# Performance work log

Measured on AMD Instinct MI355X. Metric: run time of the kernel, lower is better.

The kernel has to match this reference:

```python
import jax, jax.numpy as jnp
import numpy as np

N = 50000          # nodes
E = 1600000        # edges (avg degree 32)
IN = 256
OUT = 16
HEADS = 8
NEG_SLOPE = 0.2


def setup_inputs() -> dict:
    key = jax.random.key(0)
    k1, k2, k3, k4, k5, k6 = jax.random.split(key, 6)
    row = jax.random.randint(k1, (E,), 0, N)            # destination node of each edge
    col = jax.random.randint(k2, (E,), 0, N)            # source node of each edge
    h = jax.random.normal(k3, (N, IN), dtype=jnp.float32)
    # xavier-uniform-like scales
    w_scale = float(np.sqrt(6.0 / (IN + OUT * HEADS)))
    a_scale = float(np.sqrt(6.0 / (HEADS * OUT + 1)))
    W = jax.random.uniform(k4, (IN, OUT * HEADS), jnp.float32, -w_scale, w_scale)
    a_l = jax.random.uniform(k5, (1, HEADS, OUT), jnp.float32, -a_scale, a_scale)
    a_r = jax.random.uniform(k6, (1, HEADS, OUT), jnp.float32, -a_scale, a_scale)
    return {"row": row, "col": col, "h": h, "W": W, "a_l": a_l, "a_r": a_r}


def reference(row, col, h, W, a_l, a_r):
    n = h.shape[0]
    heads, out = a_l.shape[1], a_l.shape[2]
    Wh = (h @ W).reshape(n, heads, out)                 # [N, H, D]
    Wh1 = (Wh * a_l).sum(2)                             # [N, H]
    Wh2 = (Wh * a_r).sum(2)                             # [N, H]
    e = Wh1[row] + Wh2[col]                             # [E, H]
    e = jnp.where(e > 0, e, NEG_SLOPE * e)              # leaky relu
    # segment (row-wise) softmax over edges sharing the same destination row
    m = jax.ops.segment_max(e, row, num_segments=n)     # [N, H]
    ex = jnp.exp(e - m[row])                            # [E, H]
    s = jax.ops.segment_sum(ex, row, num_segments=n)    # [N, H]
    alpha = ex / s[row]                                 # [E, H]
    # torch .reshape(-1, out, heads) reinterprets memory layout (NOT a transpose)
    Wh_r = Wh.reshape(n, out, heads)                    # [N, D, H]
    msg = alpha[:, None, :] * Wh_r[col]                 # [E, D, H]
    h_prime = jax.ops.segment_sum(msg, row, num_segments=n)  # [N, D, H]
    return jax.nn.relu(h_prime)
```

## Files before the change

### kernel.cpp

```cpp
#include <hip/hip_runtime.h>
#include <cfloat>
#include <math.h>


constexpr int IN_F  = 256;
constexpr int F     = 128;
constexpr int HEADS = 8;
constexpr int BS    = 32;
constexpr int BSH   = 5;
constexpr int SLAB  = 2048;
constexpr int CSLAB = 9216;
constexpr int PTILE = 4096;

typedef __attribute__((ext_vector_type(8))) short bf16x8;
typedef __attribute__((ext_vector_type(4))) float f32x4;

__device__ inline uint f2bf(float x) {
    uint u = __float_as_uint(x);
    return (u + 0x7fffu + ((u >> 16) & 1u)) >> 16;
}
__device__ inline uint pack2(float a, float b) { return f2bf(a) | (f2bf(b) << 16); }

__global__ __launch_bounds__(256) void prepack(const float* __restrict__ W,
                                               uint4* __restrict__ Wf,
                                               int* __restrict__ cursorC,
                                               int* __restrict__ cursorF,
                                               int NC, int NBF)
{
    if (blockIdx.x == 0) {
        for (int i = threadIdx.x; i < NC; i += 256) cursorC[i] = i * CSLAB;
        for (int i = threadIdx.x; i < NBF; i += 256) cursorF[i] = i * SLAB;
    }
    int t = blockIdx.x * 256 + threadIdx.x;
    if (t >= 8 * 8 * 64) return;
    int ks = t >> 9, nt = (t >> 6) & 7, l = t & 63;
    int col = nt * 16 + (l & 15);
    int k0 = ks * 32 + (l >> 4) * 8;
    float v[8];
#pragma unroll
    for (int i = 0; i < 8; ++i) v[i] = W[(size_t)(k0 + i) * F + col];
    Wf[t] = make_uint4(pack2(v[0], v[1]), pack2(v[2], v[3]),
                       pack2(v[4], v[5]), pack2(v[6], v[7]));
}

__global__ __launch_bounds__(256) void gemm_push(
    const float* __restrict__ h, const uint4* __restrict__ Wf,
    const float* __restrict__ a_l, const float* __restrict__ a_r,
    uint* __restrict__ Whb, float* __restrict__ Wh1, float* __restrict__ Wh2,
    int n, int NGEMM,
    const int* __restrict__ row, const int* __restrict__ col,
    int* __restrict__ cursorC, uint* __restrict__ cpairs, int E)
{
    __shared__ uint stage[PTILE];
    __shared__ int hist[256], st[256], cur[256], gbase[256];
    const int tid = threadIdx.x;

    if (blockIdx.x >= NGEMM) {
        const int t = tid;
        const int i0 = (blockIdx.x - NGEMM) * PTILE;
        const int cnt = min(PTILE, E - i0);
        hist[t] = 0;
        __syncthreads();

        uint u[PTILE / 256];
#pragma unroll
        for (int j = 0; j < PTILE / 256; ++j) {
            const int idx = t + j * 256;
            if (idx < cnt) {
                int r = row[i0 + idx], c = col[i0 + idx];
                u[j] = ((uint)(r >> 8) << 24) | ((uint)c << 8) | (uint)(r & 255);
                atomicAdd(&hist[r >> 8], 1);
            } else u[j] = 0xFFFFFFFFu;
        }
        __syncthreads();

        const int v = hist[t];
        st[t] = v;
        __syncthreads();
        for (int off = 1; off < 256; off <<= 1) {
            int x = (t >= off) ? st[t - off] : 0;
            __syncthreads();
            st[t] += x;
            __syncthreads();
        }
        cur[t] = st[t] - v;
        if (v) gbase[t] = atomicAdd(&cursorC[t], v);
        __syncthreads();

#pragma unroll
        for (int j = 0; j < PTILE / 256; ++j) {
            if (u[j] != 0xFFFFFFFFu) {
                int k = u[j] >> 24;
                int pos = atomicAdd(&cur[k], 1);
                stage[pos] = u[j];
            }
        }
        __syncthreads();

        for (int p = t; p < cnt; p += 256) {
            uint wv = stage[p];
            int k = wv >> 24;
            int lstart = st[k] - hist[k];
            __builtin_nontemporal_store(wv & 0xFFFFFFu, &cpairs[gbase[k] + (p - lstart)]);
        }
        return;
    }

    const int w = tid >> 6, l = tid & 63;
    const int r0 = blockIdx.x * 64 + w * 16;
    const int rA = min(r0 + (l & 15), n - 1);
    const int kb = (l >> 4) * 8;

    const float* hp = &h[(size_t)rA * IN_F + kb];
    f32x4 af[16];
#pragma unroll
    for (int ks = 0; ks < 8; ++ks) {
        af[2 * ks]     = __builtin_nontemporal_load((const f32x4*)(hp + ks * 32));
        af[2 * ks + 1] = __builtin_nontemporal_load((const f32x4*)(hp + ks * 32 + 4));
    }
    uint4 Abf[8];
#pragma unroll
    for (int ks = 0; ks < 8; ++ks) {
        f32x4 a0 = af[2 * ks], a1 = af[2 * ks + 1];
        Abf[ks] = make_uint4(pack2(a0[0], a0[1]), pack2(a0[2], a0[3]),
                             pack2(a1[0], a1[1]), pack2(a1[2], a1[3]));
    }

    f32x4 acc[8];
#pragma unroll
    for (int i = 0; i < 8; ++i) acc[i] = (f32x4)0.f;

#pragma unroll
    for (int ks = 0; ks < 8; ++ks) {
        union { uint4 u; bf16x8 v; } A;
        A.u = Abf[ks];
        const uint4* wp = &Wf[ks * 512 + l];
#pragma unroll
        for (int nt = 0; nt < 8; ++nt) {
            union { uint4 u; bf16x8 v; } B;
            B.u = wp[nt * 64];
            acc[nt] = __builtin_amdgcn_mfma_f32_16x16x32_bf16(A.v, B.v, acc[nt], 0, 0, 0);
        }
    }

    const int c16 = l & 15;
    const int rowm = r0 + 4 * (l >> 4);
    float al[8], ar[8];
#pragma unroll
    for (int H = 0; H < 8; ++H) {
        al[H] = a_l[H * 16 + c16];
        ar[H] = a_r[H * 16 + c16];
    }
#pragma unroll
    for (int reg = 0; reg < 4; ++reg) {
        const int r = rowm + reg;
        float s1v[8], s2v[8];
#pragma unroll
        for (int H = 0; H < 8; ++H) {
            float wv = acc[H][reg];
            s1v[H] = wv * al[H];
            s2v[H] = wv * ar[H];
        }
#pragma unroll
        for (int d = 1; d <= 8; d <<= 1) {
#pragma unroll
            for (int H = 0; H < 8; ++H) {
                s1v[H] += __shfl_xor(s1v[H], d);
                s2v[H] += __shfl_xor(s2v[H], d);
            }
        }
        if (r < n) {
#pragma unroll
            for (int nt = 0; nt < 4; ++nt)
                Whb[(size_t)r * 64 + nt * 16 + c16] = pack2(acc[nt][reg], acc[nt + 4][reg]);
            if (c16 == 0) {
                *(float4*)&Wh1[r * 8]     = make_float4(s1v[0], s1v[1], s1v[2], s1v[3]);
                *(float4*)&Wh1[r * 8 + 4] = make_float4(s1v[4], s1v[5], s1v[6], s1v[7]);
                *(float4*)&Wh2[r * 8]     = make_float4(s2v[0], s2v[1], s2v[2], s2v[3]);
                *(float4*)&Wh2[r * 8 + 4] = make_float4(s2v[4], s2v[5], s2v[6], s2v[7]);
            }
        }
    }
}

__global__ __launch_bounds__(256) void push2_kernel(
    const uint* __restrict__ cpairs, const int* __restrict__ cursorC,
    int* __restrict__ cursorF, uint* __restrict__ pairs)
{
    __shared__ int hl[8];
    __shared__ int cur8[8];
    const int c = blockIdx.x;
    const int p0 = c * CSLAB;
    const int ec = cursorC[c] - p0;
    const int t = threadIdx.x;
    if (t < 8) hl[t] = 0;
    __syncthreads();
    for (int p = t; p < ec; p += 256)
        atomicAdd(&hl[(cpairs[p0 + p] >> 5) & 7], 1);
    __syncthreads();
    if (t < 8)
        cur8[t] = hl[t] ? atomicAdd(&cursorF[c * 8 + t], hl[t]) : 0;
    __syncthreads();
    for (int p = t; p < ec; p += 256) {
        uint u = cpairs[p0 + p];
        int pos = atomicAdd(&cur8[(u >> 5) & 7], 1);
        __builtin_nontemporal_store(((u >> 8) << 5) | (u & 31), &pairs[pos]);
    }
}

__global__ __launch_bounds__(256) void bucket_gat(
    const uint* __restrict__ pairs, const int* __restrict__ cursorF,
    const uint* __restrict__ Whb, const float* __restrict__ Wh1,
    const float* __restrict__ Wh2, float* __restrict__ out, int n)
{
    __shared__ uint cols_l[SLAB];
    __shared__ int cnt_l[BS], st0[BS], cur_l[BS];
    const int t = threadIdx.x;
    const int b = blockIdx.x;
    const int p0 = b * SLAB;
    const int ec = cursorF[b] - p0;

    if (t < BS) cnt_l[t] = 0;
    __syncthreads();
    for (int p = t; p < ec; p += 256)
        atomicAdd(&cnt_l[pairs[p0 + p] & (BS - 1)], 1);
    __syncthreads();
    if (t < BS) {
        int v = cnt_l[t];
        int inc = v;
#pragma unroll
        for (int off = 1; off < BS; off <<= 1) {
            int x = __shfl_up(inc, off);
            if (t >= off) inc += x;
        }
        st0[t] = inc - v;
        cur_l[t] = inc - v;
    }
    __syncthreads();
    for (int p = t; p < ec; p += 256) {
        uint u = pairs[p0 + p];
        int slot = atomicAdd(&cur_l[u & (BS - 1)], 1);
        cols_l[slot] = u >> BSH;
    }
    __syncthreads();

    const int wv = t >> 6, lane = t & 63;
    const int h8 = lane & 7, es = lane >> 3;
#pragma unroll 1
    for (int i = 0; i < 8; ++i) {
        const int rl = wv * 8 + i;
        const int r = (b << BSH) + rl;
        if (r >= n) continue;
        const float w1 = Wh1[r * HEADS + h8];
        const int st = st0[rl];
        const int deg = cnt_l[rl];
        if (deg == 0) {
            __builtin_nontemporal_store(0.f, &out[(size_t)r * F + lane]);
            __builtin_nontemporal_store(0.f, &out[(size_t)r * F + 64 + lane]);
            continue;
        }

        auto calc_ex = [&](int g) -> float {
            const int kk = g + es;
            const bool valid = kk < deg;
            const uint c = cols_l[st + (valid ? kk : deg - 1)];
            float e = w1 + Wh2[c * HEADS + h8];
            e = e > 0.f ? e : 0.2f * e;
            e = fminf(e, 60.f);
            return valid ? __expf(e) : 0.f;
        };

        float acc0 = 0.f, acc1 = 0.f, sm = 0.f;
        const int nfull8 = deg & ~7;
        float ex = calc_ex(0);

#pragma unroll 1
        for (int g = 0; g < nfull8; g += 8) {
            const float exn = (g + 8 < deg) ? calc_ex(g + 8) : 0.f;
            sm += ex;
#pragma unroll
            for (int k = 0; k < 8; ++k) {
                float pA = __shfl(ex, k * 8 + h8);
                uint ck = cols_l[st + g + k];
                uint wb = Whb[((size_t)ck << 6) + lane];
                acc0 = fmaf(pA, __uint_as_float(wb << 16), acc0);
                acc1 = fmaf(pA, __uint_as_float(wb & 0xffff0000u), acc1);
            }
            ex = exn;
        }
        if (nfull8 < deg) {
            sm += ex;
            const int m8 = deg - nfull8;
            for (int k = 0; k < m8; ++k) {
                float pA = __shfl(ex, k * 8 + h8);
                uint ck = cols_l[st + nfull8 + k];
                uint wb = Whb[((size_t)ck << 6) + lane];
                acc0 = fmaf(pA, __uint_as_float(wb << 16), acc0);
                acc1 = fmaf(pA, __uint_as_float(wb & 0xffff0000u), acc1);
            }
        }

        sm += __shfl_xor(sm, 8);
        sm += __shfl_xor(sm, 16);
        sm += __shfl_xor(sm, 32);
        const float inv = 1.f / sm;
        __builtin_nontemporal_store(fmaxf(acc0 * inv, 0.f), &out[(size_t)r * F + lane]);
        __builtin_nontemporal_store(fmaxf(acc1 * inv, 0.f), &out[(size_t)r * F + 64 + lane]);
    }
}

extern "C" void kernel_launch(void* const* d_in, const int* in_sizes, int n_in,
                              void* d_out, int out_size, void* d_ws, size_t ws_size,
                              hipStream_t stream)
{
    const int* row = (const int*)d_in[0];
    const int* col = (const int*)d_in[1];
    const float* h   = (const float*)d_in[2];
    const float* W   = (const float*)d_in[3];
    const float* a_l = (const float*)d_in[4];
    const float* a_r = (const float*)d_in[5];
    const int E = in_sizes[0];
    const int n = in_sizes[2] / IN_F;
    float* out = (float*)d_out;
    const int NBF = (n + BS - 1) >> BSH;
    const int NC  = (n + 255) >> 8;
    const int NGEMM = (n + 63) / 64;
    const int NPUSH = (E + PTILE - 1) / PTILE;

    char* p = (char*)d_ws;
    auto alloc = [&](size_t bytes) -> char* {
        char* q = p;
        p += (bytes + 255) & ~(size_t)255;
        return q;
    };
    uint*  Whb     = (uint*)alloc((size_t)n * 64 * 4);
    float* Wh1     = (float*)alloc((size_t)n * HEADS * 4);
    float* Wh2     = (float*)alloc((size_t)n * HEADS * 4);
    uint4* Wf      = (uint4*)alloc(8 * 8 * 64 * 16);
    int*   cursorC = (int*)alloc((size_t)NC * 4);
    int*   cursorF = (int*)alloc((size_t)NBF * 4);
    uint*  cpairs  = (uint*)alloc((size_t)NC * CSLAB * 4);
    uint*  pairs   = (uint*)alloc((size_t)NBF * SLAB * 4);

    prepack<<<16, 256, 0, stream>>>(W, Wf, cursorC, cursorF, NC, NBF);
    gemm_push<<<NGEMM + NPUSH, 256, 0, stream>>>(h, Wf, a_l, a_r, Whb, Wh1, Wh2,
                                                 n, NGEMM, row, col, cursorC, cpairs, E);
    push2_kernel<<<NC, 256, 0, stream>>>(cpairs, cursorC, cursorF, pairs);
    bucket_gat<<<NBF, 256, 0, stream>>>(pairs, cursorF, Whb, Wh1, Wh2, out, n);
}
```

Before: 138.3 us.

## Reschedule kernels: fuse push1 with prepack and overlap push2 with GEMM

The first edge-bucketing pass now runs in the same launch as the W prepack, and the second bucketing pass shares a launch with the bf16 GEMM. This cuts the four kernels to three. Cursor initialisation is replaced by memsets of count arrays, with slab bases computed inline. The aim is to hide the small push2 pass behind the GEMM and remove one launch plus its serialisation gap, at the cost of two memset operations and mixed block roles in the GEMM launch.

```diff
diff --git a/kernel.cpp b/kernel.cpp
--- a/kernel.cpp
+++ b/kernel.cpp
@@ -21,93 +21,112 @@
 }
 __device__ inline uint pack2(float a, float b) { return f2bf(a) | (f2bf(b) << 16); }
 
-__global__ __launch_bounds__(256) void prepack(const float* __restrict__ W,
-                                               uint4* __restrict__ Wf,
-                                               int* __restrict__ cursorC,
-                                               int* __restrict__ cursorF,
-                                               int NC, int NBF)
+__global__ __launch_bounds__(256) void push1_prepack(
+    const int* __restrict__ row, const int* __restrict__ col,
+    int* __restrict__ ccnt, uint* __restrict__ cpairs, int E, int NPUSH,
+    const float* __restrict__ W, uint4* __restrict__ Wf)
 {
-    if (blockIdx.x == 0) {
-        for (int i = threadIdx.x; i < NC; i += 256) cursorC[i] = i * CSLAB;
-        for (int i = threadIdx.x; i < NBF; i += 256) cursorF[i] = i * SLAB;
-    }
-    int t = blockIdx.x * 256 + threadIdx.x;
-    if (t >= 8 * 8 * 64) return;
-    int ks = t >> 9, nt = (t >> 6) & 7, l = t & 63;
-    int col = nt * 16 + (l & 15);
-    int k0 = ks * 32 + (l >> 4) * 8;
-    float v[8];
-#pragma unroll
-    for (int i = 0; i < 8; ++i) v[i] = W[(size_t)(k0 + i) * F + col];
-    Wf[t] = make_uint4(pack2(v[0], v[1]), pack2(v[2], v[3]),
-                       pack2(v[4], v[5]), pack2(v[6], v[7]));
-}
-
-__global__ __launch_bounds__(256) void gemm_push(
+    __shared__ uint stage[PTILE];
+    __shared__ int hist[256], st[256], cur[256], gbase[256];
+    const int t = threadIdx.x;
+
+    if (blockIdx.x >= NPUSH) {
+        int tt = (blockIdx.x - NPUSH) * 256 + t;
+        if (tt >= 8 * 8 * 64) return;
+        int ks = tt >> 9, nt = (tt >> 6) & 7, l = tt & 63;
+        int c = nt * 16 + (l & 15);
+        int k0 = ks * 32 + (l >> 4) * 8;
+        float v[8];
+#pragma unroll
+        for (int i = 0; i < 8; ++i) v[i] = W[(size_t)(k0 + i) * F + c];
+        Wf[tt] = make_uint4(pack2(v[0], v[1]), pack2(v[2], v[3]),
+                            pack2(v[4], v[5]), pack2(v[6], v[7]));
+        return;
+    }
+
+    const int i0 = blockIdx.x * PTILE;
+    const int cnt = min(PTILE, E - i0);
+    hist[t] = 0;
+    __syncthreads();
+
+    uint u[PTILE / 256];
+#pragma unroll
+    for (int j = 0; j < PTILE / 256; ++j) {
+        const int idx = t + j * 256;
+        if (idx < cnt) {
+            int r = row[i0 + idx], c = col[i0 + idx];
+            u[j] = ((uint)(r >> 8) << 24) | ((uint)c << 8) | (uint)(r & 255);
+            atomicAdd(&hist[r >> 8], 1);
+        } else u[j] = 0xFFFFFFFFu;
+    }
+    __syncthreads();
+
+    const int v = hist[t];
+    st[t] = v;
+    __syncthreads();
+    for (int off = 1; off < 256; off <<= 1) {
+        int x = (t >= off) ? st[t - off] : 0;
+        __syncthreads();
+        st[t] += x;
+        __syncthreads();
+    }
+    cur[t] = st[t] - v;
+    if (v) gbase[t] = t * CSLAB + atomicAdd(&ccnt[t], v);
+    __syncthreads();
+
+#pragma unroll
+    for (int j = 0; j < PTILE / 256; ++j) {
+        if (u[j] != 0xFFFFFFFFu) {
+            int k = u[j] >> 24;
+            int pos = atomicAdd(&cur[k], 1);
+            stage[pos] = u[j];
+        }
+    }
+    __syncthreads();
+
+    for (int p = t; p < cnt; p += 256) {
+        uint wv = stage[p];
+        int k = wv >> 24;
+        int lstart = st[k] - hist[k];
+        __builtin_nontemporal_store(wv & 0xFFFFFFu, &cpairs[gbase[k] + (p - lstart)]);
+    }
+}
+
+__global__ __launch_bounds__(256) void gemm_push2(
     const float* __restrict__ h, const uint4* __restrict__ Wf,
     const float* __restrict__ a_l, const float* __restrict__ a_r,
     uint* __restrict__ Whb, float* __restrict__ Wh1, float* __restrict__ Wh2,
-    int n, int NGEMM,
-    const int* __restrict__ row, const int* __restrict__ col,
-    int* __restrict__ cursorC, uint* __restrict__ cpairs, int E)
+    int n, int NC,
+    const uint* __restrict__ cpairs, const int* __restrict__ ccnt,
+    int* __restrict__ fcnt, uint* __restrict__ pairs)
 {
-    __shared__ uint stage[PTILE];
-    __shared__ int hist[256], st[256], cur[256], gbase[256];
+    __shared__ int hl[8];
+    __shared__ int cur8[8];
     const int tid = threadIdx.x;
 
-    if (blockIdx.x >= NGEMM) {
-        const int t = tid;
-        const int i0 = (blockIdx.x - NGEMM) * PTILE;
-        const int cnt = min(PTILE, E - i0);
-        hist[t] = 0;
-        __syncthreads();
-
-        uint u[PTILE / 256];
-#pragma unroll
-        for (int j = 0; j < PTILE / 256; ++j) {
-            const int idx = t + j * 256;
-            if (idx < cnt) {
-                int r = row[i0 + idx], c = col[i0 + idx];
-                u[j] = ((uint)(r >> 8) << 24) | ((uint)c << 8) | (uint)(r & 255);
-                atomicAdd(&hist[r >> 8], 1);
-            } else u[j] = 0xFFFFFFFFu;
-        }
-        __syncthreads();
-
-        const int v = hist[t];
-        st[t] = v;
-        __syncthreads();
-        for (int off = 1; off < 256; off <<= 1) {
-            int x = (t >= off) ? st[t - off] : 0;
-            __syncthreads();
-            st[t] += x;
-            __syncthreads();
-        }
-        cur[t] = st[t] - v;
-        if (v) gbase[t] = atomicAdd(&cursorC[t], v);
-        __syncthreads();
-
-#pragma unroll
-        for (int j = 0; j < PTILE / 256; ++j) {
-            if (u[j] != 0xFFFFFFFFu) {
-                int k = u[j] >> 24;
-                int pos = atomicAdd(&cur[k], 1);
-                stage[pos] = u[j];
-            }
-        }
-        __syncthreads();
-
-        for (int p = t; p < cnt; p += 256) {
-            uint wv = stage[p];
-            int k = wv >> 24;
-            int lstart = st[k] - hist[k];
-            __builtin_nontemporal_store(wv & 0xFFFFFFu, &cpairs[gbase[k] + (p - lstart)]);
+    if (blockIdx.x < NC) {
+        const int c = blockIdx.x;
+        const int p0 = c * CSLAB;
+        const int ec = ccnt[c];
+        if (tid < 8) hl[tid] = 0;
+        __syncthreads();
+        for (int p = tid; p < ec; p += 256)
+            atomicAdd(&hl[(cpairs[p0 + p] >> 5) & 7], 1);
+        __syncthreads();
+        if (tid < 8)
+            cur8[tid] = hl[tid] ? (c * 8 + tid) * SLAB + atomicAdd(&fcnt[c * 8 + tid], hl[tid]) : 0;
+        __syncthreads();
+        for (int p = tid; p < ec; p += 256) {
+            uint u = cpairs[p0 + p];
+            int pos = atomicAdd(&cur8[(u >> 5) & 7], 1);
+            __builtin_nontemporal_store(((u >> 8) << 5) | (u & 31), &pairs[pos]);
         }
         return;
     }
 
+    const int bid = blockIdx.x - NC;
     const int w = tid >> 6, l = tid & 63;
-    const int r0 = blockIdx.x * 64 + w * 16;
+    const int r0 = bid * 64 + w * 16;
     const int rA = min(r0 + (l & 15), n - 1);
     const int kb = (l >> 4) * 8;
 
@@ -183,33 +202,8 @@
     }
 }
 
-__global__ __launch_bounds__(256) void push2_kernel(
-    const uint* __restrict__ cpairs, const int* __restrict__ cursorC,
-    int* __restrict__ cursorF, uint* __restrict__ pairs)
-{
-    __shared__ int hl[8];
-    __shared__ int cur8[8];
-    const int c = blockIdx.x;
-    const int p0 = c * CSLAB;
-    const int ec = cursorC[c] - p0;
-    const int t = threadIdx.x;
-    if (t < 8) hl[t] = 0;
-    __syncthreads();
-    for (int p = t; p < ec; p += 256)
-        atomicAdd(&hl[(cpairs[p0 + p] >> 5) & 7], 1);
-    __syncthreads();
-    if (t < 8)
-        cur8[t] = hl[t] ? atomicAdd(&cursorF[c * 8 + t], hl[t]) : 0;
-    __syncthreads();
-    for (int p = t; p < ec; p += 256) {
-        uint u = cpairs[p0 + p];
-        int pos = atomicAdd(&cur8[(u >> 5) & 7], 1);
-        __builtin_nontemporal_store(((u >> 8) << 5) | (u & 31), &pairs[pos]);
-    }
-}
-
 __global__ __launch_bounds__(256) void bucket_gat(
-    const uint* __restrict__ pairs, const int* __restrict__ cursorF,
+    const uint* __restrict__ pairs, const int* __restrict__ fcnt,
     const uint* __restrict__ Whb, const float* __restrict__ Wh1,
     const float* __restrict__ Wh2, float* __restrict__ out, int n)
 {
@@ -218,7 +212,7 @@
     const int t = threadIdx.x;
     const int b = blockIdx.x;
     const int p0 = b * SLAB;
-    const int ec = cursorF[b] - p0;
+    const int ec = fcnt[b];
 
     if (t < BS) cnt_l[t] = 0;
     __syncthreads();
@@ -333,18 +327,20 @@
         p += (bytes + 255) & ~(size_t)255;
         return q;
     };
-    uint*  Whb     = (uint*)alloc((size_t)n * 64 * 4);
-    float* Wh1     = (float*)alloc((size_t)n * HEADS * 4);
-    float* Wh2     = (float*)alloc((size_t)n * HEADS * 4);
-    uint4* Wf      = (uint4*)alloc(8 * 8 * 64 * 16);
-    int*   cursorC = (int*)alloc((size_t)NC * 4);
-    int*   cursorF = (int*)alloc((size_t)NBF * 4);
-    uint*  cpairs  = (uint*)alloc((size_t)NC * CSLAB * 4);
-    uint*  pairs   = (uint*)alloc((size_t)NBF * SLAB * 4);
-
-    prepack<<<16, 256, 0, stream>>>(W, Wf, cursorC, cursorF, NC, NBF);
-    gemm_push<<<NGEMM + NPUSH, 256, 0, stream>>>(h, Wf, a_l, a_r, Whb, Wh1, Wh2,
-                                                 n, NGEMM, row, col, cursorC, cpairs, E);
-    push2_kernel<<<NC, 256, 0, stream>>>(cpairs, cursorC, cursorF, pairs);
-    bucket_gat<<<NBF, 256, 0, stream>>>(pairs, cursorF, Whb, Wh1, Wh2, out, n);
-}
+    uint*  Whb    = (uint*)alloc((size_t)n * 64 * 4);
+    float* Wh1    = (float*)alloc((size_t)n * HEADS * 4);
+    float* Wh2    = (float*)alloc((size_t)n * HEADS * 4);
+    uint4* Wf     = (uint4*)alloc(8 * 8 * 64 * 16);
+    int*   ccnt   = (int*)alloc((size_t)NC * 4);
+    int*   fcnt   = (int*)alloc((size_t)NBF * 4);
+    uint*  cpairs = (uint*)alloc((size_t)NC * CSLAB * 4);
+    uint*  pairs  = (uint*)alloc((size_t)NBF * SLAB * 4);
+
+    hipMemsetAsync(ccnt, 0, (size_t)NC * 4, stream);
+    hipMemsetAsync(fcnt, 0, (size_t)NBF * 4, stream);
+
+    push1_prepack<<<NPUSH + 16, 256, 0, stream>>>(row, col, ccnt, cpairs, E, NPUSH, W, Wf);
+    gemm_push2<<<NC + NGEMM, 256, 0, stream>>>(h, Wf, a_l, a_r, Whb, Wh1, Wh2,
+                                               n, NC, cpairs, ccnt, fcnt, pairs);
+    bucket_gat<<<NBF, 256, 0, stream>>>(pairs, fcnt, Whb, Wh1, Wh2, out, n);
+}
```

Result: faster. 133.6 us, median of 2 (-3.4%).
